# Kernel tuning notes

Measured on AMD Instinct MI355X. Metric: run time of the kernel, lower is better.

Reference implementation:

```python
import jax, jax.numpy as jnp
import numpy as np

IN_F, OUT_F, BLOCK, NBLK = 1024, 4096, 256, 16
TOPK = NBLK // 4  # 4, as in forward: n_blocks // 4


def setup_inputs() -> dict:
    key = jax.random.key(0)
    ks = jax.random.split(key, 7)
    s = 1.0 / np.sqrt(IN_F)
    s2 = 1.0 / np.sqrt(OUT_F)
    return {
        "x": jax.random.normal(ks[0], (4, 4096, IN_F), jnp.float32),
        "router_w": jax.random.uniform(ks[1], (NBLK, IN_F), jnp.float32, -s, s),
        "router_b": jax.random.uniform(ks[2], (NBLK,), jnp.float32, -s, s),
        "w1": jax.random.uniform(ks[3], (OUT_F, IN_F), jnp.float32, -s, s),
        "b1": jax.random.uniform(ks[4], (OUT_F,), jnp.float32, -s, s),
        "w2": jax.random.uniform(ks[5], (IN_F, OUT_F), jnp.float32, -s2, s2),
        "b2": jax.random.uniform(ks[6], (IN_F,), jnp.float32, -s2, s2),
    }


def reference(x, router_w, router_b, w1, b1, w2, b2):
    x_shape = x.shape
    xf = x.reshape(-1, IN_F)  # [N, d]
    n = xf.shape[0]
    # router: Linear + softmax, then top-k block selection per token
    prob = jax.nn.softmax(xf @ router_w.T + router_b, axis=-1)  # [N, n_blocks]
    _, idx = jax.lax.top_k(prob, TOPK)  # [N, k]
    mask = jnp.zeros((n, NBLK), bool).at[jnp.arange(n)[:, None], idx].set(True)
    # RoutedLinearRow: per-block fc1, zeros at unselected blocks
    w1b = w1.reshape(NBLK, BLOCK, IN_F)
    b1b = b1.reshape(NBLK, BLOCK)
    h = jnp.einsum('nd,ibd->nib', xf, w1b) + b1b  # [N, n_blocks, block]
    h = jnp.where(mask[:, :, None], h, jnp.zeros((), h.dtype))
    h = jax.nn.relu(h)
    # RoutedLinearCol: only selected blocks contribute
    w2b = w2.reshape(IN_F, NBLK, BLOCK)
    y = jnp.einsum('nib,dib->nd', jnp.where(mask[:, :, None], h, 0.0), w2b) + b2
    return y.reshape(x_shape)
```

## Files before the change

kernel.cpp:

```cpp
#include <hip/hip_runtime.h>
#include <hip/hip_bf16.h>

#define NTOK   16384
#define INF    1024
#define OUTF   4096
#define NBLK   16
#define BLKSZ  256
#define KTOP   4

typedef short bf16x8 __attribute__((ext_vector_type(8)));
typedef float f32x4 __attribute__((ext_vector_type(4)));
typedef unsigned short u16x8 __attribute__((ext_vector_type(8)));

__device__ __forceinline__ unsigned short f2bf(float f) {
  unsigned u = __float_as_uint(f);
  u += 0x7FFFu + ((u >> 16) & 1u);
  return (unsigned short)(u >> 16);
}

__device__ __forceinline__ void load_lds16(const void* g, void* l) {
  __builtin_amdgcn_global_load_lds(
      (const __attribute__((address_space(1))) unsigned int*)g,
      (__attribute__((address_space(3))) unsigned int*)l, 16, 0, 0);
}

__device__ __forceinline__ double shfl_xor_d(double v, int m) {
  long long l = __double_as_longlong(v);
  int lo = (int)(l & 0xFFFFFFFFll), hi = (int)(l >> 32);
  lo = __shfl_xor(lo, m);
  hi = __shfl_xor(hi, m);
  return __longlong_as_double(((long long)hi << 32) | (unsigned long long)(unsigned)lo);
}

__device__ __forceinline__ int pi_perm(int j) {
  return (j & 128) | ((j & 7) << 4) | ((j >> 3) & 15);
}

__global__ void k_zero(unsigned* __restrict__ list32, unsigned* __restrict__ counts) {
  int i = blockIdx.x * 256 + threadIdx.x;
  if (i < 33792) list32[i] = 0;
  else if (i < 33808) counts[i - 33792] = 0;
}

__global__ __launch_bounds__(256) void k_convert(
    const float* __restrict__ w1, const float* __restrict__ w2,
    const float* __restrict__ b1, unsigned short* __restrict__ w1b,
    unsigned short* __restrict__ w2p, float* __restrict__ b1p) {
  const size_t stride = (size_t)gridDim.x * 256;
  for (size_t i = (size_t)blockIdx.x * 256 + threadIdx.x; i < 1573376; i += stride) {
    if (i < 1048576) {
      float4 v = ((const float4*)w1)[i];
      ushort4 o;
      o.x = f2bf(v.x); o.y = f2bf(v.y); o.z = f2bf(v.z); o.w = f2bf(v.w);
      ((ushort4*)w1b)[i] = o;
    } else if (i < 1572864) {
      const size_t g = i - 1048576;
      const int d = (int)(g >> 9);
      const int rest = (int)(g & 511);
      const int jg = rest * 8;
      const int blk = jg >> 8;
      const int j0 = jg & 255;
      const float* src = w2 + (size_t)d * 4096 + blk * 256;
      u16x8 o;
#pragma unroll
      for (int ni = 0; ni < 8; ++ni) o[ni] = f2bf(src[pi_perm(j0 + ni)]);
      *(u16x8*)(w2p + (size_t)d * 4096 + jg) = o;
    } else {
      const int idx = (int)(i - 1572864);
      const int jg = idx * 8;
      const int blk = jg >> 8;
      const int j0 = jg & 255;
      const float* src = b1 + blk * 256;
      float o[8];
#pragma unroll
      for (int ni = 0; ni < 8; ++ni) o[ni] = src[pi_perm(j0 + ni)];
      float4* dst = (float4*)(b1p + jg);
      dst[0] = make_float4(o[0], o[1], o[2], o[3]);
      dst[1] = make_float4(o[4], o[5], o[6], o[7]);
    }
  }
}

__global__ __launch_bounds__(256) void k_router(
    const float* __restrict__ x, const float* __restrict__ rw,
    const float* __restrict__ rb, unsigned* __restrict__ tok_blocks,
    unsigned* __restrict__ counts, unsigned short* __restrict__ xb) {
  __shared__ float4 rwl[4096];
  const int tid = threadIdx.x;
  const float4* rw4 = (const float4*)rw;
  for (int i = tid; i < 4096; i += 256) rwl[i] = rw4[i];
  __syncthreads();

  const int n = blockIdx.x * 32 + (tid >> 3);
  const int q = tid & 7;
  double p[16];
#pragma unroll
  for (int j = 0; j < 16; ++j) p[j] = 0.0;
  const float4* xr = (const float4*)(x + (size_t)n * INF);
  ushort4* xbr = (ushort4*)(xb + (size_t)n * INF);
#pragma unroll 4
  for (int i = 0; i < 32; ++i) {
    const int d4 = q + i * 8;
    const float4 xv = xr[d4];
    ushort4 o;
    o.x = f2bf(xv.x); o.y = f2bf(xv.y); o.z = f2bf(xv.z); o.w = f2bf(xv.w);
    xbr[d4] = o;
#pragma unroll
    for (int j = 0; j < 16; ++j) {
      const float4 wv = rwl[j * 256 + d4];
      p[j] = fma((double)xv.x, (double)wv.x, p[j]);
      p[j] = fma((double)xv.y, (double)wv.y, p[j]);
      p[j] = fma((double)xv.z, (double)wv.z, p[j]);
      p[j] = fma((double)xv.w, (double)wv.w, p[j]);
    }
  }
#pragma unroll
  for (int j = 0; j < 16; ++j) {
    double v = p[j];
    v += shfl_xor_d(v, 1);
    v += shfl_xor_d(v, 2);
    v += shfl_xor_d(v, 4);
    p[j] = v + (double)rb[j];
  }

  __syncthreads();
  unsigned* hist = (unsigned*)rwl;
  if (tid < 16) hist[tid] = 0;
  __syncthreads();

  if (q == 0) {
    unsigned packed = 0;
#pragma unroll
    for (int j = 0; j < 16; ++j) {
      int r = 0;
#pragma unroll
      for (int j2 = 0; j2 < 16; ++j2)
        r += (int)((p[j2] > p[j]) | ((p[j2] == p[j]) & (j2 < j)));
      if (r < KTOP) packed |= (unsigned)j << (8 * r);
    }
    tok_blocks[n] = packed;
    atomicAdd(&hist[packed & 15u], 1u);
    atomicAdd(&hist[(packed >> 8) & 15u], 1u);
    atomicAdd(&hist[(packed >> 16) & 15u], 1u);
    atomicAdd(&hist[(packed >> 24) & 15u], 1u);
  }
  __syncthreads();
  if (tid < 16 && hist[tid]) atomicAdd(&counts[tid], hist[tid]);
}

__global__ void k_scan(const unsigned* __restrict__ counts, unsigned* __restrict__ off,
                       unsigned* __restrict__ cursors) {
  if (threadIdx.x == 0 && blockIdx.x == 0) {
    unsigned o = 0;
    for (int i = 0; i < 16; ++i) {
      off[i] = o; cursors[i] = o;
      o += (counts[i] + 127u) & ~127u;
    }
    off[16] = o;
  }
}

__global__ __launch_bounds__(256) void k_build(
    const unsigned* __restrict__ tok_blocks, unsigned* __restrict__ cursors,
    unsigned short* __restrict__ list, unsigned* __restrict__ inv) {
  const int n = blockIdx.x * 256 + threadIdx.x;
  const unsigned packed = tok_blocks[n];
  const int lane = threadIdx.x & 63;
  for (int b = 0; b < 16; ++b) {
    int r = -1;
#pragma unroll
    for (int q = 0; q < 4; ++q)
      if (((packed >> (8 * q)) & 15u) == (unsigned)b) r = q;
    unsigned long long m = __ballot(r >= 0);
    if (m) {
      int leader = __ffsll((unsigned long long)m) - 1;
      unsigned base = 0;
      if (lane == leader) base = atomicAdd(&cursors[b], (unsigned)__popcll(m));
      base = (unsigned)__shfl((int)base, leader);
      if (r >= 0) {
        unsigned pos = base + (unsigned)__popcll(m & ((1ull << lane) - 1ull));
        list[pos] = (unsigned short)n;
        inv[(size_t)n * 4 + r] = pos;
      }
    }
  }
}

__global__ __launch_bounds__(256, 2) void k_fc1(
    const unsigned short* __restrict__ xb, const unsigned short* __restrict__ w1b,
    const float* __restrict__ b1p, const unsigned short* __restrict__ list,
    const unsigned* __restrict__ counts, const unsigned* __restrict__ off,
    unsigned short* __restrict__ hg) {
  const int bid0 = blockIdx.x;
  const int bid = (bid0 & 7) * 256 + (bid0 >> 3);
  const int blk = bid >> 7;
  const int tile = bid & 127;
  const unsigned cnt = counts[blk];
  if ((unsigned)(tile * 128) >= cnt) return;
  const unsigned goff = off[blk] + tile * 128;

  __shared__ __align__(16) unsigned short As[128 * 64];
  __shared__ __align__(16) unsigned short Bs[256 * 64];
  __shared__ unsigned toks[128];

  const int tid = threadIdx.x;
  const int lane = tid & 63;
  const int wid = tid >> 6;
  const int wr = wid >> 1, wc = wid & 1;

  if (tid < 128) toks[tid] = list[goff + tid];
  __syncthreads();

  unsigned tokr[4]; int arow[4];
#pragma unroll
  for (int r = 0; r < 4; ++r) { arow[r] = (r * 256 + tid) >> 3; tokr[r] = toks[arow[r]]; }
  const int asl = tid & 7;

  f32x4 acc[4][8] = {};

  for (int k0 = 0; k0 < 1024; k0 += 64) {
    __syncthreads();
#pragma unroll
    for (int r = 0; r < 4; ++r) {
      const int kcs = asl ^ (arow[r] & 7);
      load_lds16(xb + (size_t)tokr[r] * INF + k0 + kcs * 8,
                 (char*)As + (r * 256 + wid * 64) * 16);
    }
#pragma unroll
    for (int r = 0; r < 8; ++r) {
      const int row = (r * 256 + tid) >> 3;
      const int kcs = asl ^ (row & 7);
      load_lds16(w1b + ((size_t)(blk * 256 + row)) * INF + k0 + kcs * 8,
                 (char*)Bs + (r * 256 + wid * 64) * 16);
    }
    __syncthreads();
#pragma unroll
    for (int ks = 0; ks < 2; ++ks) {
      bf16x8 a[4], b[8];
#pragma unroll
      for (int mi = 0; mi < 4; ++mi) {
        const int row = wr * 64 + mi * 16 + (lane & 15);
        const int kc = ks * 4 + (lane >> 4);
        a[mi] = *(const bf16x8*)((const char*)As + row * 128 + ((kc ^ (row & 7)) << 4));
      }
#pragma unroll
      for (int ni = 0; ni < 8; ++ni) {
        const int row = wc * 128 + ni * 16 + (lane & 15);
        const int kc = ks * 4 + (lane >> 4);
        b[ni] = *(const bf16x8*)((const char*)Bs + row * 128 + ((kc ^ (row & 7)) << 4));
      }
#pragma unroll
      for (int mi = 0; mi < 4; ++mi)
#pragma unroll
        for (int ni = 0; ni < 8; ++ni)
          acc[mi][ni] = __builtin_amdgcn_mfma_f32_16x16x32_bf16(a[mi], b[ni], acc[mi][ni], 0, 0, 0);
    }
  }
  const int c16 = lane & 15;
  const float4* bp = (const float4*)(b1p + blk * 256 + wc * 128 + c16 * 8);
  const float4 bv0 = bp[0], bv1 = bp[1];
  const float bvv[8] = {bv0.x, bv0.y, bv0.z, bv0.w, bv1.x, bv1.y, bv1.z, bv1.w};
#pragma unroll
  for (int mi = 0; mi < 4; ++mi) {
#pragma unroll
    for (int i = 0; i < 4; ++i) {
      const int row = wr * 64 + mi * 16 + (lane >> 4) * 4 + i;
      u16x8 w;
#pragma unroll
      for (int ni = 0; ni < 8; ++ni) {
        float v = acc[mi][ni][i] + bvv[ni];
        v = v > 0.f ? v : 0.f;
        w[ni] = f2bf(v);
      }
      *(u16x8*)(hg + (size_t)(goff + row) * 256 + wc * 128 + c16 * 8) = w;
    }
  }
}

__global__ __launch_bounds__(256, 2) void k_fc2(
    const unsigned short* __restrict__ hg, const unsigned short* __restrict__ w2p,
    const unsigned* __restrict__ counts, const unsigned* __restrict__ off,
    unsigned short* __restrict__ part) {
  const int bid0 = blockIdx.x;
  const int bid = (bid0 & 7) * 256 + (bid0 >> 3);
  const int blk = bid >> 7;
  const int tile = bid & 127;
  const unsigned cnt = counts[blk];
  if ((unsigned)(tile * 128) >= cnt) return;
  const unsigned goff = off[blk] + tile * 128;
  const int rem = (int)cnt - tile * 128;

  __shared__ __align__(16) unsigned short As[128 * 64];
  __shared__ __align__(16) unsigned short Bs[256 * 64];

  const int tid = threadIdx.x;
  const int lane = tid & 63;
  const int wid = tid >> 6;
  const int wr = wid >> 1, wc = wid & 1;
  const int asl = tid & 7;
  const int c16 = lane & 15;

  for (int ns = 0; ns < 4; ++ns) {
    f32x4 acc[4][8] = {};
    for (int k0 = 0; k0 < 256; k0 += 64) {
      __syncthreads();
#pragma unroll
      for (int r = 0; r < 4; ++r) {
        const int row = (r * 256 + tid) >> 3;
        const int kcs = asl ^ (row & 7);
        load_lds16(hg + (size_t)(goff + row) * BLKSZ + k0 + kcs * 8,
                   (char*)As + (r * 256 + wid * 64) * 16);
      }
#pragma unroll
      for (int r = 0; r < 8; ++r) {
        const int row = (r * 256 + tid) >> 3;
        const int kcs = asl ^ (row & 7);
        load_lds16(w2p + (size_t)(ns * 256 + row) * OUTF + blk * 256 + k0 + kcs * 8,
                   (char*)Bs + (r * 256 + wid * 64) * 16);
      }
      __syncthreads();
#pragma unroll
      for (int ks = 0; ks < 2; ++ks) {
        bf16x8 a[4], b[8];
#pragma unroll
        for (int mi = 0; mi < 4; ++mi) {
          const int row = wr * 64 + mi * 16 + (lane & 15);
          const int kc = ks * 4 + (lane >> 4);
          a[mi] = *(const bf16x8*)((const char*)As + row * 128 + ((kc ^ (row & 7)) << 4));
        }
#pragma unroll
        for (int ni = 0; ni < 8; ++ni) {
          const int row = wc * 128 + ni * 16 + (lane & 15);
          const int kc = ks * 4 + (lane >> 4);
          b[ni] = *(const bf16x8*)((const char*)Bs + row * 128 + ((kc ^ (row & 7)) << 4));
        }
#pragma unroll
        for (int mi = 0; mi < 4; ++mi)
#pragma unroll
          for (int ni = 0; ni < 8; ++ni)
            acc[mi][ni] = __builtin_amdgcn_mfma_f32_16x16x32_bf16(a[mi], b[ni], acc[mi][ni], 0, 0, 0);
      }
    }
#pragma unroll
    for (int mi = 0; mi < 4; ++mi) {
#pragma unroll
      for (int i = 0; i < 4; ++i) {
        const int mrow = wr * 64 + mi * 16 + (lane >> 4) * 4 + i;
        if (mrow < rem) {
          u16x8 w;
#pragma unroll
          for (int ni = 0; ni < 8; ++ni) w[ni] = f2bf(acc[mi][ni][i]);
          *(u16x8*)(part + (size_t)(goff + mrow) * 1024 + ns * 256 + wc * 128 + c16 * 8) = w;
        }
      }
    }
  }
}

__global__ __launch_bounds__(256) void k_reduce(const unsigned short* __restrict__ part,
                                                const unsigned* __restrict__ inv,
                                                const float* __restrict__ b2,
                                                float* __restrict__ out) {
  __shared__ float lds[8 * 1028];
  const int tid = threadIdx.x;
  const int tok0 = blockIdx.x * 8;
  const int tok_l = tid >> 5;
  const int l32 = tid & 31;

  const uint4 iv = *(const uint4*)(inv + (size_t)(tok0 + tok_l) * 4);
  const unsigned prow[4] = {iv.x, iv.y, iv.z, iv.w};

#pragma unroll
  for (int g = 0; g < 4; ++g) {
    const int idx = g * 32 + l32;
    const int p0 = idx * 8;
    float s[8] = {0.f, 0.f, 0.f, 0.f, 0.f, 0.f, 0.f, 0.f};
#pragma unroll
    for (int sl = 0; sl < 4; ++sl) {
      u16x8 v = *(const u16x8*)(part + (size_t)prow[sl] * 1024 + p0);
#pragma unroll
      for (int j = 0; j < 8; ++j)
        s[j] += __uint_as_float((unsigned)(unsigned short)v[j] << 16);
    }
    const int ns = idx >> 5, wcb = (idx >> 4) & 1, cc = idx & 15;
#pragma unroll
    for (int ni = 0; ni < 8; ++ni)
      lds[tok_l * 1028 + ns * 256 + wcb * 128 + ni * 16 + cc] = s[ni];
  }
  __syncthreads();
  const float4 b2v = ((const float4*)b2)[tid];
#pragma unroll
  for (int r = 0; r < 8; ++r) {
    f32x4 lv = *(f32x4*)&lds[r * 1028 + tid * 4];
    float4 o = make_float4(lv[0] + b2v.x, lv[1] + b2v.y, lv[2] + b2v.z, lv[3] + b2v.w);
    *(float4*)(out + (size_t)(tok0 + r) * 1024 + tid * 4) = o;
  }
}

extern "C" void kernel_launch(void* const* d_in, const int* in_sizes, int n_in,
                              void* d_out, int out_size, void* d_ws, size_t ws_size,
                              hipStream_t stream) {
  const float* x  = (const float*)d_in[0];
  const float* rw = (const float*)d_in[1];
  const float* rb = (const float*)d_in[2];
  const float* w1 = (const float*)d_in[3];
  const float* b1 = (const float*)d_in[4];
  const float* w2 = (const float*)d_in[5];
  const float* b2 = (const float*)d_in[6];
  float* out = (float*)d_out;

  char* ws = (char*)d_ws;
  unsigned short* part = (unsigned short*)(ws);
  unsigned short* xb   = (unsigned short*)(ws);
  unsigned short* w1b  = (unsigned short*)(ws + 33554432);
  unsigned short* hg   = (unsigned short*)(ws + 138412032);
  unsigned short* w2p  = (unsigned short*)(ws + 173015040);
  unsigned* tokb       = (unsigned*)(ws + 181403648);
  unsigned short* list = (unsigned short*)(ws + 181469184);
  unsigned* inv        = (unsigned*)(ws + 181604352);
  float* b1p           = (float*)(ws + 181866496);
  unsigned* counts     = (unsigned*)(ws + 181882880);
  unsigned* off        = (unsigned*)(ws + 181882944);
  unsigned* cursors    = (unsigned*)(ws + 181883072);

  k_zero<<<dim3(133), dim3(256), 0, stream>>>((unsigned*)list, counts);
  k_convert<<<dim3(1024), dim3(256), 0, stream>>>(w1, w2, b1, w1b, w2p, b1p);
  k_router<<<dim3(512), dim3(256), 0, stream>>>(x, rw, rb, tokb, counts, xb);
  k_scan<<<dim3(1), dim3(64), 0, stream>>>(counts, off, cursors);
  k_build<<<dim3(64), dim3(256), 0, stream>>>(tokb, cursors, list, inv);
  k_fc1<<<dim3(2048), dim3(256), 0, stream>>>(xb, w1b, b1p, list, counts, off, hg);
  k_fc2<<<dim3(2048), dim3(256), 0, stream>>>(hg, w2p, counts, off, part);
  k_reduce<<<dim3(2048), dim3(256), 0, stream>>>(part, inv, b2, out);
}
```

Baseline: 316.5 us.

## Fuse fc1 and fc2 into one kernel keeping hidden tile in LDS

Merges the two routed GEMM kernels into a single 512-thread kernel that computes the fc1 tile, applies bias and ReLU, and stores the bf16 hidden activations into a swizzled LDS buffer. fc2 then reads them from LDS instead of a global hg buffer. This removes the global write and read of the hidden activations and one kernel launch. In exchange it uses a large LDS allocation at one block per CU, and each wave now holds a smaller accumulator tile. The workspace layout is reshuffled, so xb no longer aliases part, and the rem guard on partial tiles is dropped.

After: 292.5 us. 7.6% less time.

```diff
diff --git a/kernel.cpp b/kernel.cpp
--- a/kernel.cpp
+++ b/kernel.cpp
@@ -186,11 +186,17 @@
   }
 }
 
-__global__ __launch_bounds__(256, 2) void k_fc1(
+__global__ __launch_bounds__(512, 1) void k_ffn(
     const unsigned short* __restrict__ xb, const unsigned short* __restrict__ w1b,
-    const float* __restrict__ b1p, const unsigned short* __restrict__ list,
-    const unsigned* __restrict__ counts, const unsigned* __restrict__ off,
-    unsigned short* __restrict__ hg) {
+    const unsigned short* __restrict__ w2p, const float* __restrict__ b1p,
+    const unsigned short* __restrict__ list, const unsigned* __restrict__ counts,
+    const unsigned* __restrict__ off, unsigned short* __restrict__ part) {
+  __shared__ __align__(16) char lds[114688];
+  char* As  = lds + 65536;
+  char* Bs  = lds + 81920;
+  char* Bs2 = lds + 65536;
+  __shared__ unsigned toks[128];
+
   const int bid0 = blockIdx.x;
   const int bid = (bid0 & 7) * 256 + (bid0 >> 3);
   const int blk = bid >> 7;
@@ -199,159 +205,128 @@
   if ((unsigned)(tile * 128) >= cnt) return;
   const unsigned goff = off[blk] + tile * 128;
 
-  __shared__ __align__(16) unsigned short As[128 * 64];
-  __shared__ __align__(16) unsigned short Bs[256 * 64];
-  __shared__ unsigned toks[128];
-
   const int tid = threadIdx.x;
   const int lane = tid & 63;
   const int wid = tid >> 6;
-  const int wr = wid >> 1, wc = wid & 1;
+  const int wr = wid >> 1;
+  const int wc = wid & 1;
+  const int asl = tid & 7;
+  const int c16 = lane & 15;
 
   if (tid < 128) toks[tid] = list[goff + tid];
   __syncthreads();
 
-  unsigned tokr[4]; int arow[4];
-#pragma unroll
-  for (int r = 0; r < 4; ++r) { arow[r] = (r * 256 + tid) >> 3; tokr[r] = toks[arow[r]]; }
-  const int asl = tid & 7;
-
-  f32x4 acc[4][8] = {};
-
+  const unsigned tok0 = toks[tid >> 3];
+  const unsigned tok1 = toks[64 + (tid >> 3)];
+
+  f32x4 acc[2][8] = {};
   for (int k0 = 0; k0 < 1024; k0 += 64) {
-    __syncthreads();
+    {
+      const int row0 = tid >> 3;
+      const int kcs0 = asl ^ (row0 & 7);
+      load_lds16(xb + (size_t)tok0 * INF + k0 + kcs0 * 8, As + (wid * 64) * 16);
+      const int row1 = 64 + row0;
+      const int kcs1 = asl ^ (row1 & 7);
+      load_lds16(xb + (size_t)tok1 * INF + k0 + kcs1 * 8, As + (512 + wid * 64) * 16);
+    }
 #pragma unroll
     for (int r = 0; r < 4; ++r) {
-      const int kcs = asl ^ (arow[r] & 7);
-      load_lds16(xb + (size_t)tokr[r] * INF + k0 + kcs * 8,
-                 (char*)As + (r * 256 + wid * 64) * 16);
-    }
-#pragma unroll
-    for (int r = 0; r < 8; ++r) {
-      const int row = (r * 256 + tid) >> 3;
+      const int row = (r * 512 + tid) >> 3;
       const int kcs = asl ^ (row & 7);
       load_lds16(w1b + ((size_t)(blk * 256 + row)) * INF + k0 + kcs * 8,
-                 (char*)Bs + (r * 256 + wid * 64) * 16);
+                 Bs + (r * 512 + wid * 64) * 16);
     }
     __syncthreads();
 #pragma unroll
     for (int ks = 0; ks < 2; ++ks) {
-      bf16x8 a[4], b[8];
-#pragma unroll
-      for (int mi = 0; mi < 4; ++mi) {
-        const int row = wr * 64 + mi * 16 + (lane & 15);
-        const int kc = ks * 4 + (lane >> 4);
-        a[mi] = *(const bf16x8*)((const char*)As + row * 128 + ((kc ^ (row & 7)) << 4));
+      const int kc = ks * 4 + (lane >> 4);
+      bf16x8 a[2], b[8];
+#pragma unroll
+      for (int mi = 0; mi < 2; ++mi) {
+        const int row = wr * 32 + mi * 16 + (lane & 15);
+        a[mi] = *(const bf16x8*)(As + row * 128 + ((kc ^ (row & 7)) << 4));
       }
 #pragma unroll
       for (int ni = 0; ni < 8; ++ni) {
         const int row = wc * 128 + ni * 16 + (lane & 15);
-        const int kc = ks * 4 + (lane >> 4);
-        b[ni] = *(const bf16x8*)((const char*)Bs + row * 128 + ((kc ^ (row & 7)) << 4));
-      }
-#pragma unroll
-      for (int mi = 0; mi < 4; ++mi)
+        b[ni] = *(const bf16x8*)(Bs + row * 128 + ((kc ^ (row & 7)) << 4));
+      }
+#pragma unroll
+      for (int mi = 0; mi < 2; ++mi)
 #pragma unroll
         for (int ni = 0; ni < 8; ++ni)
           acc[mi][ni] = __builtin_amdgcn_mfma_f32_16x16x32_bf16(a[mi], b[ni], acc[mi][ni], 0, 0, 0);
     }
-  }
-  const int c16 = lane & 15;
-  const float4* bp = (const float4*)(b1p + blk * 256 + wc * 128 + c16 * 8);
-  const float4 bv0 = bp[0], bv1 = bp[1];
-  const float bvv[8] = {bv0.x, bv0.y, bv0.z, bv0.w, bv1.x, bv1.y, bv1.z, bv1.w};
-#pragma unroll
-  for (int mi = 0; mi < 4; ++mi) {
-#pragma unroll
-    for (int i = 0; i < 4; ++i) {
-      const int row = wr * 64 + mi * 16 + (lane >> 4) * 4 + i;
-      u16x8 w;
-#pragma unroll
-      for (int ni = 0; ni < 8; ++ni) {
-        float v = acc[mi][ni][i] + bvv[ni];
-        v = v > 0.f ? v : 0.f;
-        w[ni] = f2bf(v);
-      }
-      *(u16x8*)(hg + (size_t)(goff + row) * 256 + wc * 128 + c16 * 8) = w;
-    }
-  }
-}
-
-__global__ __launch_bounds__(256, 2) void k_fc2(
-    const unsigned short* __restrict__ hg, const unsigned short* __restrict__ w2p,
-    const unsigned* __restrict__ counts, const unsigned* __restrict__ off,
-    unsigned short* __restrict__ part) {
-  const int bid0 = blockIdx.x;
-  const int bid = (bid0 & 7) * 256 + (bid0 >> 3);
-  const int blk = bid >> 7;
-  const int tile = bid & 127;
-  const unsigned cnt = counts[blk];
-  if ((unsigned)(tile * 128) >= cnt) return;
-  const unsigned goff = off[blk] + tile * 128;
-  const int rem = (int)cnt - tile * 128;
-
-  __shared__ __align__(16) unsigned short As[128 * 64];
-  __shared__ __align__(16) unsigned short Bs[256 * 64];
-
-  const int tid = threadIdx.x;
-  const int lane = tid & 63;
-  const int wid = tid >> 6;
-  const int wr = wid >> 1, wc = wid & 1;
-  const int asl = tid & 7;
-  const int c16 = lane & 15;
+    __syncthreads();
+  }
+
+  {
+    const float4* bp = (const float4*)(b1p + blk * 256 + wc * 128 + c16 * 8);
+    const float4 bv0 = bp[0], bv1 = bp[1];
+    const float bvv[8] = {bv0.x, bv0.y, bv0.z, bv0.w, bv1.x, bv1.y, bv1.z, bv1.w};
+    const int chunk = wc * 16 + c16;
+    const int cslot = (chunk & ~7);
+    const int clow  = (chunk & 7);
+#pragma unroll
+    for (int mi = 0; mi < 2; ++mi) {
+#pragma unroll
+      for (int i = 0; i < 4; ++i) {
+        const int row = wr * 32 + mi * 16 + (lane >> 4) * 4 + i;
+        u16x8 wv;
+#pragma unroll
+        for (int ni = 0; ni < 8; ++ni) {
+          float v = acc[mi][ni][i] + bvv[ni];
+          v = v > 0.f ? v : 0.f;
+          wv[ni] = f2bf(v);
+        }
+        *(u16x8*)(lds + row * 512 + ((cslot | (clow ^ (row & 7))) << 4)) = wv;
+      }
+    }
+  }
+  __syncthreads();
 
   for (int ns = 0; ns < 4; ++ns) {
-    f32x4 acc[4][8] = {};
+    f32x4 acc2[2][8] = {};
     for (int k0 = 0; k0 < 256; k0 += 64) {
-      __syncthreads();
 #pragma unroll
       for (int r = 0; r < 4; ++r) {
-        const int row = (r * 256 + tid) >> 3;
-        const int kcs = asl ^ (row & 7);
-        load_lds16(hg + (size_t)(goff + row) * BLKSZ + k0 + kcs * 8,
-                   (char*)As + (r * 256 + wid * 64) * 16);
-      }
-#pragma unroll
-      for (int r = 0; r < 8; ++r) {
-        const int row = (r * 256 + tid) >> 3;
+        const int row = (r * 512 + tid) >> 3;
         const int kcs = asl ^ (row & 7);
         load_lds16(w2p + (size_t)(ns * 256 + row) * OUTF + blk * 256 + k0 + kcs * 8,
-                   (char*)Bs + (r * 256 + wid * 64) * 16);
+                   Bs2 + (r * 512 + wid * 64) * 16);
       }
       __syncthreads();
 #pragma unroll
       for (int ks = 0; ks < 2; ++ks) {
-        bf16x8 a[4], b[8];
-#pragma unroll
-        for (int mi = 0; mi < 4; ++mi) {
-          const int row = wr * 64 + mi * 16 + (lane & 15);
-          const int kc = ks * 4 + (lane >> 4);
-          a[mi] = *(const bf16x8*)((const char*)As + row * 128 + ((kc ^ (row & 7)) << 4));
+        const int kc = ks * 4 + (lane >> 4);
+        bf16x8 a[2], b[8];
+#pragma unroll
+        for (int mi = 0; mi < 2; ++mi) {
+          const int row = wr * 32 + mi * 16 + (lane & 15);
+          a[mi] = *(const bf16x8*)(lds + row * 512 + k0 * 2 + ((kc ^ (row & 7)) << 4));
         }
 #pragma unroll
         for (int ni = 0; ni < 8; ++ni) {
           const int row = wc * 128 + ni * 16 + (lane & 15);
-          const int kc = ks * 4 + (lane >> 4);
-          b[ni] = *(const bf16x8*)((const char*)Bs + row * 128 + ((kc ^ (row & 7)) << 4));
+          b[ni] = *(const bf16x8*)(Bs2 + row * 128 + ((kc ^ (row & 7)) << 4));
         }
 #pragma unroll
-        for (int mi = 0; mi < 4; ++mi)
+        for (int mi = 0; mi < 2; ++mi)
 #pragma unroll
           for (int ni = 0; ni < 8; ++ni)
-            acc[mi][ni] = __builtin_amdgcn_mfma_f32_16x16x32_bf16(a[mi], b[ni], acc[mi][ni], 0, 0, 0);
-      }
-    }
-#pragma unroll
-    for (int mi = 0; mi < 4; ++mi) {
+            acc2[mi][ni] = __builtin_amdgcn_mfma_f32_16x16x32_bf16(a[mi], b[ni], acc2[mi][ni], 0, 0, 0);
+      }
+      __syncthreads();
+    }
+#pragma unroll
+    for (int mi = 0; mi < 2; ++mi) {
 #pragma unroll
       for (int i = 0; i < 4; ++i) {
-        const int mrow = wr * 64 + mi * 16 + (lane >> 4) * 4 + i;
-        if (mrow < rem) {
-          u16x8 w;
-#pragma unroll
-          for (int ni = 0; ni < 8; ++ni) w[ni] = f2bf(acc[mi][ni][i]);
-          *(u16x8*)(part + (size_t)(goff + mrow) * 1024 + ns * 256 + wc * 128 + c16 * 8) = w;
-        }
+        const int row = wr * 32 + mi * 16 + (lane >> 4) * 4 + i;
+        u16x8 wv;
+#pragma unroll
+        for (int ni = 0; ni < 8; ++ni) wv[ni] = f2bf(acc2[mi][ni][i]);
+        *(u16x8*)(part + (size_t)(goff + row) * 1024 + ns * 256 + wc * 128 + c16 * 8) = wv;
       }
     }
   }
@@ -411,24 +386,22 @@
 
   char* ws = (char*)d_ws;
   unsigned short* part = (unsigned short*)(ws);
-  unsigned short* xb   = (unsigned short*)(ws);
-  unsigned short* w1b  = (unsigned short*)(ws + 33554432);
-  unsigned short* hg   = (unsigned short*)(ws + 138412032);
-  unsigned short* w2p  = (unsigned short*)(ws + 173015040);
-  unsigned* tokb       = (unsigned*)(ws + 181403648);
-  unsigned short* list = (unsigned short*)(ws + 181469184);
-  unsigned* inv        = (unsigned*)(ws + 181604352);
-  float* b1p           = (float*)(ws + 181866496);
-  unsigned* counts     = (unsigned*)(ws + 181882880);
-  unsigned* off        = (unsigned*)(ws + 181882944);
-  unsigned* cursors    = (unsigned*)(ws + 181883072);
+  unsigned short* xb   = (unsigned short*)(ws + 138412032);
+  unsigned short* w1b  = (unsigned short*)(ws + 171966464);
+  unsigned short* w2p  = (unsigned short*)(ws + 180355072);
+  unsigned* tokb       = (unsigned*)(ws + 188743680);
+  unsigned short* list = (unsigned short*)(ws + 188809216);
+  unsigned* inv        = (unsigned*)(ws + 188944384);
+  float* b1p           = (float*)(ws + 189206528);
+  unsigned* counts     = (unsigned*)(ws + 189222912);
+  unsigned* off        = (unsigned*)(ws + 189222976);
+  unsigned* cursors    = (unsigned*)(ws + 189223104);
 
   k_zero<<<dim3(133), dim3(256), 0, stream>>>((unsigned*)list, counts);
   k_convert<<<dim3(1024), dim3(256), 0, stream>>>(w1, w2, b1, w1b, w2p, b1p);
   k_router<<<dim3(512), dim3(256), 0, stream>>>(x, rw, rb, tokb, counts, xb);
   k_scan<<<dim3(1), dim3(64), 0, stream>>>(counts, off, cursors);
   k_build<<<dim3(64), dim3(256), 0, stream>>>(tokb, cursors, list, inv);
-  k_fc1<<<dim3(2048), dim3(256), 0, stream>>>(xb, w1b, b1p, list, counts, off, hg);
-  k_fc2<<<dim3(2048), dim3(256), 0, stream>>>(hg, w2p, counts, off, part);
+  k_ffn<<<dim3(2048), dim3(512), 0, stream>>>(xb, w1b, w2p, b1p, list, counts, off, part);
   k_reduce<<<dim3(2048), dim3(256), 0, stream>>>(part, inv, b2, out);
 }
```
